# Performance work log

Hardware: AMD Instinct MI355X
Metric: run time of the kernel (lower is better)

Reference implementation:

```python
import math
import jax, jax.numpy as jnp
import numpy as np

B, N, M = 8, 2048, 1024
INPUT_SIZE = 512
HEAD_DIM = 64
NUM_HEADS = 6
ATTN_SIZE = HEAD_DIM * NUM_HEADS
MAX_CLASSES = 512


def setup_inputs() -> dict:
    key = jax.random.key(0)
    k1, k2, k3, k4, k5, k6, k7 = jax.random.split(key, 7)
    bound = 1.0 / math.sqrt(INPUT_SIZE)
    return {
        "train_embeddings": jax.random.normal(k1, (B, N, INPUT_SIZE), jnp.float32),
        "test_embeddings": jax.random.normal(k2, (B, M, INPUT_SIZE), jnp.float32),
        "targets": jax.random.randint(k3, (B, N), 0, MAX_CLASSES),
        # torch nn.Linear weights, stored as [in, out] for direct matmul
        "Wq": jax.random.uniform(k4, (INPUT_SIZE, ATTN_SIZE), jnp.float32, -bound, bound),
        "bq": jax.random.uniform(k5, (ATTN_SIZE,), jnp.float32, -bound, bound),
        "Wk": jax.random.uniform(k6, (INPUT_SIZE, ATTN_SIZE), jnp.float32, -bound, bound),
        "bk": jax.random.uniform(k7, (ATTN_SIZE,), jnp.float32, -bound, bound),
    }


def reference(train_embeddings, test_embeddings, targets, Wq, bq, Wk, bk):
    b, m, _ = test_embeddings.shape
    # projections -> [B, S, H, D]
    q_bmhd = (test_embeddings @ Wq + bq).reshape(b, m, NUM_HEADS, HEAD_DIM)
    k_bnhd = (train_embeddings @ Wk + bk).reshape(b, -1, NUM_HEADS, HEAD_DIM)
    scale = 1.0 / math.sqrt(HEAD_DIM)  # SDPA default scale
    # attention scores [B, H, M, N]
    scores = jnp.einsum("bmhd,bnhd->bhmn", q_bmhd, k_bnhd) * scale
    attn = jax.nn.softmax(scores, axis=-1)
    # one-hot train targets [B, N, C]; chunk-folding in the torch code is a
    # memory trick — mathematically it is just attn @ one_hot per head
    onehot_bnc = jax.nn.one_hot(targets, MAX_CLASSES, dtype=q_bmhd.dtype)
    out_bhmc = jnp.einsum("bhmn,bnc->bhmc", attn, onehot_bnc)
    out_bmc = out_bhmc.mean(axis=1)          # mean over heads
    out_mbc = out_bmc.transpose(1, 0, 2)      # [M, B, C]
    return jnp.log(jnp.clip(out_mbc, 1e-05) + 3e-05)
```

## Files before the change

### kernel.cpp

```cpp
#include <hip/hip_runtime.h>
#include <hip/hip_bf16.h>

#define BQ 8
#define NN 2048
#define MM 1024
#define EE 512
#define NH 6
#define AA 384
#define CC 512

#define KROW_B (AA * 2)
#define TILE_B (16 * KROW_B)
#define STILE_B (32 * KROW_B)
#define WROW_B (EE * 2)
#define WTILE_B (16 * WROW_B)

#define QSCALE 0.1803368801111204f

typedef __bf16 bf16x8 __attribute__((ext_vector_type(8)));
typedef float  f32x4  __attribute__((ext_vector_type(4)));
typedef float  f32x2  __attribute__((ext_vector_type(2)));
using bf16 = __hip_bfloat16;

static __device__ __forceinline__ f32x4 mfma16(bf16x8 a, bf16x8 b, f32x4 c) {
  return __builtin_amdgcn_mfma_f32_16x16x32_bf16(a, b, c, 0, 0, 0);
}

typedef __attribute__((address_space(1))) const void gconst_void;
typedef __attribute__((address_space(3))) void lds_void_t;
static __device__ __forceinline__ void ld_lds16(const void* g, void* l) {
  __builtin_amdgcn_global_load_lds((gconst_void*)g, (lds_void_t*)l, 16, 0, 0);
}

static __device__ __forceinline__ unsigned enc_fp8(float f) {
  unsigned b = __float_as_uint(f) + 0x00080000u;
  int e = (int)((b >> 23) & 0xFF) - 120;
  if (e <= 0) return 0u;
  if (e >= 16) return 0x7Eu;
  return ((unsigned)e << 3) | ((b >> 20) & 7u);
}
static __device__ __forceinline__ float dec_fp8(unsigned u) {
  unsigned e = (u >> 3) & 0xFu;
  if (e == 0) return 0.f;
  return __uint_as_float(((e + 120u) << 23) | ((u & 7u) << 20));
}
static __device__ __forceinline__ unsigned pk4(float a, float b, float c, float d) {
#if __has_builtin(__builtin_amdgcn_cvt_pk_fp8_f32)
  int v = __builtin_amdgcn_cvt_pk_fp8_f32(a, b, 0, false);
  v = __builtin_amdgcn_cvt_pk_fp8_f32(c, d, v, true);
  return (unsigned)v;
#else
  return enc_fp8(a) | (enc_fp8(b) << 8) | (enc_fp8(c) << 16) | (enc_fp8(d) << 24);
#endif
}
static __device__ __forceinline__ unsigned pk2(float a, float b) {
#if __has_builtin(__builtin_amdgcn_cvt_pk_fp8_f32)
  return (unsigned)__builtin_amdgcn_cvt_pk_fp8_f32(a, b, 0, false);
#else
  return enc_fp8(a) | (enc_fp8(b) << 8);
#endif
}
template <bool HI>
static __device__ __forceinline__ f32x2 upk2(unsigned d) {
#if __has_builtin(__builtin_amdgcn_cvt_pk_f32_fp8)
  return __builtin_amdgcn_cvt_pk_f32_fp8((int)d, HI);
#else
  f32x2 r;
  r[0] = dec_fp8((d >> (HI ? 16 : 0)) & 0xFFu);
  r[1] = dec_fp8((d >> (HI ? 24 : 8)) & 0xFFu);
  return r;
#endif
}

__global__ __launch_bounds__(512) void prep_kernel(
    const float* __restrict__ Wq, const float* __restrict__ Wk,
    bf16* __restrict__ WqT, bf16* __restrict__ WkT,
    const int* __restrict__ targets, int* __restrict__ cnts, int* __restrict__ idxT)
{
  __shared__ float t[64][65];
  __shared__ int cnt[CC], pos[CC];
  int bid = blockIdx.x, tid = threadIdx.x;
  if (bid < 96) {
    if (tid >= 256) { __syncthreads(); return; }
    int id = bid;
    const float* W = (id < 48) ? Wq : Wk;
    bf16* WT = (id < 48) ? WqT : WkT;
    if (id >= 48) id -= 48;
    int kb = (id / 6) * 64, nb = (id % 6) * 64;
    int lr = tid >> 4, lc = (tid & 15) * 4;
    #pragma unroll
    for (int p = 0; p < 4; p++) {
      int k = lr + p * 16;
      float4 v = *reinterpret_cast<const float4*>(W + (size_t)(kb + k) * AA + nb + lc);
      t[k][lc] = v.x; t[k][lc + 1] = v.y; t[k][lc + 2] = v.z; t[k][lc + 3] = v.w;
    }
    __syncthreads();
    #pragma unroll
    for (int p = 0; p < 4; p++) {
      int n = lr + p * 16;
      bf16* dst = WT + (size_t)(nb + n) * EE + kb + lc;
      dst[0] = __float2bfloat16(t[lc][n]);
      dst[1] = __float2bfloat16(t[lc + 1][n]);
      dst[2] = __float2bfloat16(t[lc + 2][n]);
      dst[3] = __float2bfloat16(t[lc + 3][n]);
    }
    return;
  }
  int b = bid - 96;
  cnt[tid] = 0;
  pos[tid] = 0;
  #pragma unroll
  for (int s = 0; s < 32; s++) idxT[((size_t)b * 32 + s) * CC + tid] = NN;
  __syncthreads();
  int tv[4];
  #pragma unroll
  for (int i = 0; i < 4; i++) {
    tv[i] = targets[b * NN + tid * 4 + i];
    atomicAdd(&cnt[tv[i]], 1);
  }
  __syncthreads();
  cnts[b * CC + tid] = cnt[tid];
  __syncthreads();
  #pragma unroll
  for (int i = 0; i < 4; i++) {
    int p = atomicAdd(&pos[tv[i]], 1);
    if (p < 32) idxT[((size_t)b * 32 + p) * CC + tv[i]] = tid * 4 + i;
  }
}

__global__ __launch_bounds__(256, 3) void proj_kernel(
    const float* __restrict__ test, const float* __restrict__ train,
    const bf16* __restrict__ WqT, const bf16* __restrict__ WkT,
    const float* __restrict__ bq, const float* __restrict__ bk,
    bf16* __restrict__ Qb, bf16* __restrict__ Kb)
{
  __shared__ char wbuf[3][WTILE_B];
  int tid = threadIdx.x, wid = tid >> 6, lane = tid & 63;
  int bid = blockIdx.x;
  int sub = bid & 1, unit = bid >> 1;
  const float* A; const bf16* WT; const float* bias; bf16* C; float scale; int m0;
  if (unit < 128) { A = test;  WT = WqT; bias = bq; C = Qb; scale = QSCALE; m0 = unit * 64; }
  else            { A = train; WT = WkT; bias = bk; C = Kb; scale = 1.0f;   m0 = (unit - 128) * 64; }
  m0 += wid * 16;
  int row = lane & 15, hi = lane >> 4;

  bf16x8 af[16];
  const float* arow = A + (size_t)(m0 + row) * EE + hi * 8;
  #pragma unroll
  for (int ks = 0; ks < 16; ks++) {
    float4 u = *reinterpret_cast<const float4*>(arow + ks * 32);
    float4 v = *reinterpret_cast<const float4*>(arow + ks * 32 + 4);
    bf16x8 f;
    f[0] = (__bf16)u.x; f[1] = (__bf16)u.y; f[2] = (__bf16)u.z; f[3] = (__bf16)u.w;
    f[4] = (__bf16)v.x; f[5] = (__bf16)v.y; f[6] = (__bf16)v.z; f[7] = (__bf16)v.w;
    af[ks] = f;
  }

  int ldso[4], srco[4];
  #pragma unroll
  for (int i = 0; i < 4; i++) {
    int off = tid * 16 + i * 4096;
    int rw = off >> 10, c = off & 1023;
    ldso[i] = off;
    srco[i] = rw * WROW_B + (c ^ ((rw & 7) << 4));
  }
  const char* wgbase = (const char*)WT + (size_t)sub * 12 * WTILE_B;
  int sw = (row & 7) << 4;

  auto stage = [&](int t, int buf) {
    const char* src = wgbase + (size_t)t * WTILE_B;
    #pragma unroll
    for (int i = 0; i < 4; i++) ld_lds16(src + srco[i], wbuf[buf] + ldso[i]);
  };
  auto compute = [&](int buf, int t) {
    const char* wb = wbuf[buf] + row * WROW_B;
    f32x4 acc0 = {0.f, 0.f, 0.f, 0.f}, acc1 = {0.f, 0.f, 0.f, 0.f};
    #pragma unroll
    for (int ks = 0; ks < 16; ks += 2) {
      bf16x8 w0 = *reinterpret_cast<const bf16x8*>(wb + ((hi * 16 + ks * 64) ^ sw));
      bf16x8 w1 = *reinterpret_cast<const bf16x8*>(wb + ((hi * 16 + (ks + 1) * 64) ^ sw));
      acc0 = mfma16(af[ks], w0, acc0);
      acc1 = mfma16(af[ks + 1], w1, acc1);
    }
    f32x4 acc = acc0 + acc1;
    int ocol = (sub * 12 + t) * 16 + row;
    float bv = bias[ocol];
    #pragma unroll
    for (int j = 0; j < 4; j++)
      C[(size_t)(m0 + hi * 4 + j) * AA + ocol] = __float2bfloat16((acc[j] + bv) * scale);
  };

  stage(0, 0);
  stage(1, 1);
  asm volatile("s_waitcnt vmcnt(4)" ::: "memory");
  __builtin_amdgcn_s_barrier();
  __builtin_amdgcn_sched_barrier(0);
  stage(2, 2);
  compute(0, 0);

  int cur = 1, stg = 0;
  #pragma unroll 1
  for (int t = 1; t < 11; t++) {
    asm volatile("s_waitcnt vmcnt(8)" ::: "memory");
    __builtin_amdgcn_s_barrier();
    __builtin_amdgcn_sched_barrier(0);
    if (t < 10) stage(t + 2, stg);
    compute(cur, t);
    cur = cur + 1 < 3 ? cur + 1 : 0;
    stg = stg + 1 < 3 ? stg + 1 : 0;
  }
  asm volatile("s_waitcnt vmcnt(4)" ::: "memory");
  __builtin_amdgcn_s_barrier();
  __builtin_amdgcn_sched_barrier(0);
  compute(cur, 11);
}

__global__ __launch_bounds__(256, 2) void spass_kernel(
    const bf16* __restrict__ Qb, const bf16* __restrict__ Kb, char* __restrict__ Wh)
{
  __shared__ char kbuf[2][STILE_B];
  int id = blockIdx.x;
  int b = id & 7, r = id >> 3, mt = r & 7, nc = r >> 3;
  int tid = threadIdx.x, wid = tid >> 6, lane = tid & 63;
  int m0 = mt * 128 + wid * 32, n0 = nc * 256;
  int row = lane & 15, hi = lane >> 4;

  bf16x8 qf[2][12];
  #pragma unroll
  for (int s = 0; s < 2; s++) {
    const bf16* qrow = Qb + ((size_t)(b * MM + m0 + s * 16 + row)) * AA + hi * 8;
    #pragma unroll
    for (int ks = 0; ks < 12; ks++) qf[s][ks] = *reinterpret_cast<const bf16x8*>(qrow + ks * 32);
  }

  int ldso[6], srco[6];
  #pragma unroll
  for (int i = 0; i < 6; i++) {
    int off = tid * 16 + i * 4096;
    int rw = off / KROW_B, c = off - rw * KROW_B;
    ldso[i] = off;
    srco[i] = rw * KROW_B + (c ^ ((rw & 7) << 4));
  }
  const char* kgbase = (const char*)(Kb + ((size_t)(b * NN + n0)) * AA);

  int sw = (row & 7) << 4;
  int rbase = row * KROW_B;
  int x0 = rbase + ((hi * 16) ^ sw);
  int x1 = rbase + (((hi * 16) + 64) ^ sw);

  auto stage = [&](int t, int buf) {
    const char* src = kgbase + (size_t)t * STILE_B;
    #pragma unroll
    for (int i = 0; i < 6; i++) ld_lds16(src + srco[i], kbuf[buf] + ldso[i]);
  };
  auto compute = [&](int buf, int st) {
    #pragma unroll
    for (int sub = 0; sub < 2; sub++) {
      const char* kb = kbuf[buf] + sub * TILE_B;
      float w[2][NH][4];
      __builtin_amdgcn_s_setprio(1);
      #pragma unroll
      for (int h = 0; h < NH; h++) {
        bf16x8 k0 = *reinterpret_cast<const bf16x8*>(kb + h * 128 + x0);
        bf16x8 k1 = *reinterpret_cast<const bf16x8*>(kb + h * 128 + x1);
        f32x4 a0 = {0.f, 0.f, 0.f, 0.f}, a1 = {0.f, 0.f, 0.f, 0.f};
        a0 = mfma16(qf[0][2 * h], k0, a0);
        a1 = mfma16(qf[1][2 * h], k0, a1);
        a0 = mfma16(qf[0][2 * h + 1], k1, a0);
        a1 = mfma16(qf[1][2 * h + 1], k1, a1);
        #pragma unroll
        for (int j = 0; j < 4; j++) {
          w[0][h][j] = __builtin_amdgcn_exp2f(a0[j]);
          w[1][h][j] = __builtin_amdgcn_exp2f(a1[j]);
        }
      }
      __builtin_amdgcn_s_setprio(0);
      int n = n0 + (st * 2 + sub) * 16 + row;
      #pragma unroll
      for (int s = 0; s < 2; s++)
        #pragma unroll
        for (int j = 0; j < 4; j++) {
          unsigned d0 = pk4(w[s][0][j], w[s][1][j], w[s][2][j], w[s][3][j]);
          unsigned d1 = pk2(w[s][4][j], w[s][5][j]);
          int m = m0 + s * 16 + hi * 4 + j;
          *reinterpret_cast<uint2*>(Wh + (((size_t)(b * MM + m)) * NN + n) * 8) = make_uint2(d0, d1);
        }
    }
  };

  stage(0, 0);
  asm volatile("s_waitcnt vmcnt(0)" ::: "memory");
  __builtin_amdgcn_s_barrier();
  __builtin_amdgcn_sched_barrier(0);
  stage(1, 1);
  compute(0, 0);

  #pragma unroll 1
  for (int i = 1; i < 8; i++) {
    asm volatile("s_waitcnt vmcnt(16)" ::: "memory");
    __builtin_amdgcn_s_barrier();
    __builtin_amdgcn_sched_barrier(0);
    if (i < 7) stage(i + 1, (i + 1) & 1);
    compute(i & 1, i);
  }
}

__global__ __launch_bounds__(512) void gather_kernel(
    const char* __restrict__ Wh, const int* __restrict__ cnts,
    const int* __restrict__ idxT, float* __restrict__ out)
{
  __shared__ char lds[65536];
  uint2* wl = (uint2*)lds;
  int id = blockIdx.x;
  int b = id & 7, mt = id >> 3;
  int m0 = mt * 4;
  int tid = threadIdx.x, wid = tid >> 6, lane = tid & 63;
  int c = tid;

  int s8[8];
  #pragma unroll
  for (int i = 0; i < 8; i++) s8[i] = idxT[((size_t)b * 32 + i) * CC + c];
  int kc = min(cnts[b * CC + c], 32);

  const char* src = Wh + ((size_t)(b * MM + m0)) * (NN * 8);
  #pragma unroll
  for (int i = 0; i < 8; i++)
    ld_lds16(src + tid * 16 + i * 8192, lds + tid * 16 + i * 8192);
  asm volatile("s_waitcnt vmcnt(0)" ::: "memory");
  __syncthreads();

  float B[4][NH];
  #pragma unroll
  for (int m = 0; m < 4; m++)
    #pragma unroll
    for (int h = 0; h < NH; h++) B[m][h] = 0.f;

  auto accum = [&](int idx) {
    int ok = (idx < NN) ? ~0 : 0;
    int ix = idx & (NN - 1);
    #pragma unroll
    for (int m = 0; m < 4; m++) {
      uint2 u = wl[m * NN + ix];
      u.x &= (unsigned)ok; u.y &= (unsigned)ok;
      f32x2 p0 = upk2<false>(u.x);
      f32x2 p1 = upk2<true>(u.x);
      f32x2 p2 = upk2<false>(u.y);
      B[m][0] += p0[0]; B[m][1] += p0[1];
      B[m][2] += p1[0]; B[m][3] += p1[1];
      B[m][4] += p2[0]; B[m][5] += p2[1];
    }
  };
  #pragma unroll
  for (int i = 0; i < 8; i++) accum(s8[i]);
  #pragma unroll 1
  for (int i = 8; i < kc; i++)
    accum(idxT[((size_t)b * 32 + i) * CC + c]);

  __syncthreads();
  float* wred = (float*)lds;
  float* rzs  = (float*)(lds + 8 * 24 * 4);

  #pragma unroll
  for (int m = 0; m < 4; m++)
    #pragma unroll
    for (int h = 0; h < NH; h++) {
      float t = B[m][h];
      t += __shfl_xor(t, 1);  t += __shfl_xor(t, 2);  t += __shfl_xor(t, 4);
      t += __shfl_xor(t, 8);  t += __shfl_xor(t, 16); t += __shfl_xor(t, 32);
      if (lane == 0) wred[wid * 24 + m * NH + h] = t;
    }
  __syncthreads();
  if (tid < 24) {
    float z = 0.f;
    #pragma unroll
    for (int w = 0; w < 8; w++) z += wred[w * 24 + tid];
    rzs[tid] = 1.0f / (6.0f * z);
  }
  __syncthreads();

  #pragma unroll
  for (int m = 0; m < 4; m++) {
    float v = 0.f;
    #pragma unroll
    for (int h = 0; h < NH; h++) v += B[m][h] * rzs[m * NH + h];
    out[((size_t)(m0 + m) * BQ + b) * CC + c] = __logf(fmaxf(v, 1e-5f) + 3e-5f);
  }
}

extern "C" void kernel_launch(void* const* d_in, const int* in_sizes, int n_in,
                              void* d_out, int out_size, void* d_ws, size_t ws_size,
                              hipStream_t stream) {
  const float* train = (const float*)d_in[0];
  const float* test  = (const float*)d_in[1];
  const int*   tgt   = (const int*)d_in[2];
  const float* Wq    = (const float*)d_in[3];
  const float* bq    = (const float*)d_in[4];
  const float* Wk    = (const float*)d_in[5];
  const float* bk    = (const float*)d_in[6];
  float* out = (float*)d_out;

  char* ws = (char*)d_ws;
  bf16*  WqT  = (bf16*)(ws);
  bf16*  WkT  = (bf16*)(ws + 393216);
  bf16*  Qb   = (bf16*)(ws + 786432);
  bf16*  Kb   = (bf16*)(ws + 7077888);
  char*  Wh   = (char*)(ws + 19660800);
  int*   cnts = (int*)(ws + 153878528);
  int*   idxT = (int*)(ws + 153894912);

  prep_kernel<<<104, 512, 0, stream>>>(Wq, Wk, WqT, WkT, tgt, cnts, idxT);
  proj_kernel<<<768, 256, 0, stream>>>(test, train, WqT, WkT, bq, bk, Qb, Kb);
  spass_kernel<<<512, 256, 0, stream>>>(Qb, Kb, Wh);
  gather_kernel<<<2048, 512, 0, stream>>>(Wh, cnts, idxT, out);
}
```

Baseline: 118.8 us.

## Sort train rows by class so gather reads contiguous per-class ranges

The prep kernel now builds a counting sort of train indices by target class, using a prefix scan to produce per-class offsets and a permutation. The projection kernel gathers train rows through this permutation, so K and the scores come out in class-sorted order. Each class's contributions then sit in one contiguous range, and the gather kernel reads them straight from global memory instead of first staging into LDS and doing indirect lookups. The gather kernel also handles 8 test rows per block instead of 4. The trade-offs are extra scan barriers in prep, indirect row loads in the projection, and uneven per-thread loop lengths in the gather.

```diff
diff --git a/kernel.cpp b/kernel.cpp
--- a/kernel.cpp
+++ b/kernel.cpp
@@ -75,13 +75,13 @@
 __global__ __launch_bounds__(512) void prep_kernel(
     const float* __restrict__ Wq, const float* __restrict__ Wk,
     bf16* __restrict__ WqT, bf16* __restrict__ WkT,
-    const int* __restrict__ targets, int* __restrict__ cnts, int* __restrict__ idxT)
+    const int* __restrict__ targets, int* __restrict__ offs, int* __restrict__ idxs)
 {
   __shared__ float t[64][65];
-  __shared__ int cnt[CC], pos[CC];
+  __shared__ int cnt[CC], ssum[CC], pos[CC];
   int bid = blockIdx.x, tid = threadIdx.x;
   if (bid < 96) {
-    if (tid >= 256) { __syncthreads(); return; }
+    if (tid >= 256) { __syncthreads(); __syncthreads(); return; }
     int id = bid;
     const float* W = (id < 48) ? Wq : Wk;
     bf16* WT = (id < 48) ? WqT : WkT;
@@ -104,13 +104,11 @@
       dst[2] = __float2bfloat16(t[lc + 2][n]);
       dst[3] = __float2bfloat16(t[lc + 3][n]);
     }
+    __syncthreads();
     return;
   }
   int b = bid - 96;
   cnt[tid] = 0;
-  pos[tid] = 0;
-  #pragma unroll
-  for (int s = 0; s < 32; s++) idxT[((size_t)b * 32 + s) * CC + tid] = NN;
   __syncthreads();
   int tv[4];
   #pragma unroll
@@ -119,12 +117,23 @@
     atomicAdd(&cnt[tv[i]], 1);
   }
   __syncthreads();
-  cnts[b * CC + tid] = cnt[tid];
+  ssum[tid] = cnt[tid];
+  __syncthreads();
+  for (int d = 1; d < CC; d <<= 1) {
+    int v = (tid >= d) ? ssum[tid - d] : 0;
+    __syncthreads();
+    ssum[tid] += v;
+    __syncthreads();
+  }
+  int excl = ssum[tid] - cnt[tid];
+  offs[b * (CC + 1) + tid] = excl;
+  if (tid == CC - 1) offs[b * (CC + 1) + CC] = NN;
+  pos[tid] = excl;
   __syncthreads();
   #pragma unroll
   for (int i = 0; i < 4; i++) {
     int p = atomicAdd(&pos[tv[i]], 1);
-    if (p < 32) idxT[((size_t)b * 32 + p) * CC + tv[i]] = tid * 4 + i;
+    idxs[b * NN + p] = tid * 4 + i;
   }
 }
 
@@ -132,20 +141,30 @@
     const float* __restrict__ test, const float* __restrict__ train,
     const bf16* __restrict__ WqT, const bf16* __restrict__ WkT,
     const float* __restrict__ bq, const float* __restrict__ bk,
+    const int* __restrict__ idxs,
     bf16* __restrict__ Qb, bf16* __restrict__ Kb)
 {
   __shared__ char wbuf[3][WTILE_B];
   int tid = threadIdx.x, wid = tid >> 6, lane = tid & 63;
   int bid = blockIdx.x;
   int sub = bid & 1, unit = bid >> 1;
-  const float* A; const bf16* WT; const float* bias; bf16* C; float scale; int m0;
-  if (unit < 128) { A = test;  WT = WqT; bias = bq; C = Qb; scale = QSCALE; m0 = unit * 64; }
-  else            { A = train; WT = WkT; bias = bk; C = Kb; scale = 1.0f;   m0 = (unit - 128) * 64; }
-  m0 += wid * 16;
+  const bf16* WT; const float* bias; bf16* C; float scale; int m0;
+  const float* arow;
   int row = lane & 15, hi = lane >> 4;
+  if (unit < 128) {
+    WT = WqT; bias = bq; C = Qb; scale = QSCALE; m0 = unit * 64 + wid * 16;
+    arow = test + (size_t)(m0 + row) * EE + hi * 8;
+  } else {
+    WT = WkT; bias = bk; C = Kb; scale = 1.0f;
+    int g0 = (unit - 128) * 64 + wid * 16;
+    m0 = g0;
+    int g = g0 + row;
+    int b = g >> 11, pos = g & (NN - 1);
+    int srcrow = idxs[b * NN + pos];
+    arow = train + ((size_t)b * NN + srcrow) * EE + hi * 8;
+  }
 
   bf16x8 af[16];
-  const float* arow = A + (size_t)(m0 + row) * EE + hi * 8;
   #pragma unroll
   for (int ks = 0; ks < 16; ks++) {
     float4 u = *reinterpret_cast<const float4*>(arow + ks * 32);
@@ -306,80 +325,63 @@
 }
 
 __global__ __launch_bounds__(512) void gather_kernel(
-    const char* __restrict__ Wh, const int* __restrict__ cnts,
-    const int* __restrict__ idxT, float* __restrict__ out)
+    const char* __restrict__ Wh, const int* __restrict__ offs, float* __restrict__ out)
 {
-  __shared__ char lds[65536];
-  uint2* wl = (uint2*)lds;
+  __shared__ float wred[8][48];
+  __shared__ float rzs[48];
   int id = blockIdx.x;
   int b = id & 7, mt = id >> 3;
-  int m0 = mt * 4;
+  int m0 = mt * 8;
   int tid = threadIdx.x, wid = tid >> 6, lane = tid & 63;
   int c = tid;
 
-  int s8[8];
-  #pragma unroll
-  for (int i = 0; i < 8; i++) s8[i] = idxT[((size_t)b * 32 + i) * CC + c];
-  int kc = min(cnts[b * CC + c], 32);
-
-  const char* src = Wh + ((size_t)(b * MM + m0)) * (NN * 8);
-  #pragma unroll
-  for (int i = 0; i < 8; i++)
-    ld_lds16(src + tid * 16 + i * 8192, lds + tid * 16 + i * 8192);
-  asm volatile("s_waitcnt vmcnt(0)" ::: "memory");
-  __syncthreads();
-
-  float B[4][NH];
-  #pragma unroll
-  for (int m = 0; m < 4; m++)
+  int o0 = offs[b * (CC + 1) + c];
+  int o1 = offs[b * (CC + 1) + c + 1];
+  const char* rbase = Wh + ((size_t)(b * MM + m0)) * (NN * 8);
+
+  float B[8][NH];
+  #pragma unroll
+  for (int m = 0; m < 8; m++)
     #pragma unroll
     for (int h = 0; h < NH; h++) B[m][h] = 0.f;
 
-  auto accum = [&](int idx) {
-    int ok = (idx < NN) ? ~0 : 0;
-    int ix = idx & (NN - 1);
-    #pragma unroll
-    for (int m = 0; m < 4; m++) {
-      uint2 u = wl[m * NN + ix];
-      u.x &= (unsigned)ok; u.y &= (unsigned)ok;
-      f32x2 p0 = upk2<false>(u.x);
-      f32x2 p1 = upk2<true>(u.x);
-      f32x2 p2 = upk2<false>(u.y);
+  #pragma unroll 1
+  for (int i = o0; i < o1; i++) {
+    uint2 u[8];
+    #pragma unroll
+    for (int m = 0; m < 8; m++)
+      u[m] = *reinterpret_cast<const uint2*>(rbase + (size_t)m * (NN * 8) + (size_t)i * 8);
+    #pragma unroll
+    for (int m = 0; m < 8; m++) {
+      f32x2 p0 = upk2<false>(u[m].x);
+      f32x2 p1 = upk2<true>(u[m].x);
+      f32x2 p2 = upk2<false>(u[m].y);
       B[m][0] += p0[0]; B[m][1] += p0[1];
       B[m][2] += p1[0]; B[m][3] += p1[1];
       B[m][4] += p2[0]; B[m][5] += p2[1];
     }
-  };
-  #pragma unroll
-  for (int i = 0; i < 8; i++) accum(s8[i]);
-  #pragma unroll 1
-  for (int i = 8; i < kc; i++)
-    accum(idxT[((size_t)b * 32 + i) * CC + c]);
-
-  __syncthreads();
-  float* wred = (float*)lds;
-  float* rzs  = (float*)(lds + 8 * 24 * 4);
-
-  #pragma unroll
-  for (int m = 0; m < 4; m++)
+  }
+
+  #pragma unroll
+  for (int m = 0; m < 8; m++)
     #pragma unroll
     for (int h = 0; h < NH; h++) {
       float t = B[m][h];
       t += __shfl_xor(t, 1);  t += __shfl_xor(t, 2);  t += __shfl_xor(t, 4);
       t += __shfl_xor(t, 8);  t += __shfl_xor(t, 16); t += __shfl_xor(t, 32);
-      if (lane == 0) wred[wid * 24 + m * NH + h] = t;
-    }
-  __syncthreads();
-  if (tid < 24) {
+      if (lane == 0) wred[wid][m * NH + h] = t;
+    }
+  __syncthreads();
+  if (tid < 48) {
     float z = 0.f;
     #pragma unroll
-    for (int w = 0; w < 8; w++) z += wred[w * 24 + tid];
+    for (int w = 0; w < 8; w++) z += wred[w][tid];
     rzs[tid] = 1.0f / (6.0f * z);
   }
   __syncthreads();
 
   #pragma unroll
-  for (int m = 0; m < 4; m++) {
+  for (int m = 0; m < 8; m++) {
     float v = 0.f;
     #pragma unroll
     for (int h = 0; h < NH; h++) v += B[m][h] * rzs[m * NH + h];
@@ -405,11 +407,11 @@
   bf16*  Qb   = (bf16*)(ws + 786432);
   bf16*  Kb   = (bf16*)(ws + 7077888);
   char*  Wh   = (char*)(ws + 19660800);
-  int*   cnts = (int*)(ws + 153878528);
-  int*   idxT = (int*)(ws + 153894912);
-
-  prep_kernel<<<104, 512, 0, stream>>>(Wq, Wk, WqT, WkT, tgt, cnts, idxT);
-  proj_kernel<<<768, 256, 0, stream>>>(test, train, WqT, WkT, bq, bk, Qb, Kb);
+  int*   offs = (int*)(ws + 153878528);
+  int*   idxs = (int*)(ws + 153894944);
+
+  prep_kernel<<<104, 512, 0, stream>>>(Wq, Wk, WqT, WkT, tgt, offs, idxs);
+  proj_kernel<<<768, 256, 0, stream>>>(test, train, WqT, WkT, bq, bk, idxs, Qb, Kb);
   spass_kernel<<<512, 256, 0, stream>>>(Qb, Kb, Wh);
-  gather_kernel<<<2048, 512, 0, stream>>>(Wh, cnts, idxT, out);
-}
+  gather_kernel<<<1024, 512, 0, stream>>>(Wh, offs, out);
+}
```

New measurement: 209.0 us. 1.76x slower.
